# Performance work log

Hardware: AMD Instinct MI355X
Metric: run time of the kernel (lower is better)

The kernel has to match this reference:

```python
import jax, jax.numpy as jnp
import numpy as np

B = 4
MAX_N = 2048
D = 512
H = 8
HD = D // H
SRC_LENS = [2048, 1536, 1800, 1200]   # sum = 6584
REF_LENS = [1900, 2048, 1400, 1600]   # sum = 6948
NEG_INF = -1e9


def setup_inputs() -> dict:
    key = jax.random.key(0)
    ks = jax.random.split(key, 8)
    n_src, n_ref = sum(SRC_LENS), sum(REF_LENS)
    s = 0.02
    return {
        "feats_src": jax.random.normal(ks[0], (n_src, D), dtype=jnp.float32),
        "batch_src": jnp.asarray(np.repeat(np.arange(B), SRC_LENS), dtype=jnp.int32),
        "feats_ref": jax.random.normal(ks[1], (n_ref, D), dtype=jnp.float32),
        "batch_ref": jnp.asarray(np.repeat(np.arange(B), REF_LENS), dtype=jnp.int32),
        "w_in": jax.random.normal(ks[2], (3 * D, D), dtype=jnp.float32) * s,
        "b_in": jnp.zeros((3 * D,), dtype=jnp.float32),
        "w_out": jax.random.normal(ks[3], (D, D), dtype=jnp.float32) * s,
        "b_out": jnp.zeros((D,), dtype=jnp.float32),
        "gw1": jax.random.normal(ks[4], (D, D), dtype=jnp.float32) * s,
        "gb1": jnp.zeros((D,), dtype=jnp.float32),
        "gw2": jax.random.normal(ks[5], (1, D), dtype=jnp.float32) * s,
        "gb2": jnp.zeros((1,), dtype=jnp.float32),
    }


def _to_dense(feats, batch_idx):
    # sparse [N, D] (sorted batch indices) -> dense [B, MAX_N, D] + key_padding_mask
    n = feats.shape[0]
    counts = jax.ops.segment_sum(jnp.ones((n,), jnp.int32), batch_idx, num_segments=B)
    starts = jnp.concatenate([jnp.zeros((1,), jnp.int32), jnp.cumsum(counts)[:-1].astype(jnp.int32)])
    pos = jnp.arange(n, dtype=jnp.int32) - starts[batch_idx]  # position within batch
    dense = jnp.zeros((B, MAX_N, feats.shape[1]), feats.dtype).at[batch_idx, pos].set(feats)
    mask = jnp.arange(MAX_N)[None, :] >= counts[:, None]  # True = padding (key_padding_mask)
    return dense, mask, pos


def reference(feats_src, batch_src, feats_ref, batch_ref,
              w_in, b_in, w_out, b_out, gw1, gb1, gw2, gb2):
    d_src, mask_src, pos_src = _to_dense(feats_src, batch_src)
    d_ref, mask_ref, _ = _to_dense(feats_ref, batch_ref)

    # nn.MultiheadAttention (batch_first, eval mode): packed in_proj, scaled dot-product
    q = (d_src @ w_in[:D].T + b_in[:D]).reshape(B, MAX_N, H, HD)
    k = (d_ref @ w_in[D:2 * D].T + b_in[D:2 * D]).reshape(B, MAX_N, H, HD)
    v = (d_ref @ w_in[2 * D:].T + b_in[2 * D:]).reshape(B, MAX_N, H, HD)
    scores = jnp.einsum('bqhd,bkhd->bhqk', q * (HD ** -0.5), k)
    scores = jnp.where(mask_ref[:, None, None, :], NEG_INF, scores)
    attn = jax.nn.softmax(scores, axis=-1)
    ctx = jnp.einsum('bhqk,bkhd->bqhd', attn, v).reshape(B, MAX_N, D)
    d_aligned = ctx @ w_out.T + b_out

    # gate MLP: Linear -> ReLU -> Linear -> Sigmoid
    gate = jax.nn.sigmoid(jax.nn.relu(d_aligned @ gw1.T + gb1) @ gw2.T + gb2)  # [B, MAX_N, 1]
    d_out = d_src + gate * d_aligned

    # dense -> ragged: gather each token back to its flat slot
    out_flat = d_out[batch_src, pos_src]  # [N_src, D]
    return out_flat, gate
```

## Files before the change

### kernel.cpp

```cpp
#include <hip/hip_runtime.h>
#include <hip/hip_bf16.h>


typedef __bf16 bf16x8_t __attribute__((ext_vector_type(8)));
typedef __bf16 bf16x4_t __attribute__((ext_vector_type(4)));
typedef float f32x4_t __attribute__((ext_vector_type(4)));
typedef float f32x2_t __attribute__((ext_vector_type(2)));

__device__ inline bf16x8_t zero8() {
  bf16x8_t z;
#pragma unroll
  for (int t = 0; t < 8; ++t) z[t] = (__bf16)0.0f;
  return z;
}

__device__ __forceinline__ int sniff_f32(const void* w) {
  unsigned short u = ((const unsigned short*)w)[threadIdx.x & 63];
  return __ballot((u & 0x7F80) >= 0x3F80) != 0ULL;
}

__global__ void sentinel_k(float* out) {
  if (threadIdx.x == 0 && blockIdx.x == 0) out[0] = 1000.0f;
}

__global__ void cv_all(const void* w_in, const void* b_in, const void* w_out,
                       const void* b_out, const void* gw1, const void* gb1,
                       const void* gw2, const void* gb2,
                       __hip_bfloat16* __restrict__ ws) {
  int f = sniff_f32(w_in);
  const size_t F_W_IN = 16, F_B_IN = 786448, F_W_OUT = 787984, F_B_OUT = 1050128,
               F_GW1 = 1050640, F_GB1 = 1312784, F_GW2 = 1313296, F_GB2 = 1313808;
  const int total = 1313793;
  for (int g = blockIdx.x * 256 + threadIdx.x; g < total; g += gridDim.x * 256) {
    const void* src;
    size_t dst;
    int i;
    if (g < 786432) { src = w_in; dst = F_W_IN; i = g; }
    else if (g < 787968) { src = b_in; dst = F_B_IN; i = g - 786432; }
    else if (g < 1050112) { src = w_out; dst = F_W_OUT; i = g - 787968; }
    else if (g < 1050624) { src = b_out; dst = F_B_OUT; i = g - 1050112; }
    else if (g < 1312768) { src = gw1; dst = F_GW1; i = g - 1050624; }
    else if (g < 1313280) { src = gb1; dst = F_GB1; i = g - 1312768; }
    else if (g < 1313792) { src = gw2; dst = F_GW2; i = g - 1313280; }
    else { src = gb2; dst = F_GB2; i = g - 1313792; }
    ws[dst + i] = f ? __float2bfloat16(((const float*)src)[i])
                    : ((const __hip_bfloat16*)src)[i];
  }
}

template <bool AF32>
__global__ __launch_bounds__(256) void gemm128(
    const void* __restrict__ A_, long aoff, const __hip_bfloat16* __restrict__ Bt,
    const __hip_bfloat16* __restrict__ bias, __hip_bfloat16* __restrict__ C,
    int M, int K, int lda, int ldb, int ldc, float cscale, int relu,
    const void* snf) {
  __shared__ __bf16 As[128][64];
  __shared__ __bf16 Bs[128][64];
  int f = 0;
  if constexpr (AF32) f = sniff_f32(snf);
  int tid = threadIdx.x, lane = tid & 63, wave = tid >> 6;
  int wm = wave >> 1, wn = wave & 1;
  int l15 = lane & 15, quad = lane >> 4;
  int bm = blockIdx.x * 128, bn = blockIdx.y * 128;

  f32x4_t acc[4][4];
#pragma unroll
  for (int i = 0; i < 4; ++i)
#pragma unroll
    for (int j = 0; j < 4; ++j)
#pragma unroll
      for (int r = 0; r < 4; ++r) acc[i][j][r] = 0.f;

  bf16x8_t ra[4], rb[4];
  f32x4_t raf[4][2];

  auto gload = [&](int k0) {
#pragma unroll
    for (int s = 0; s < 4; ++s) {
      int id = s * 256 + tid;
      int row = id >> 3, col = (id & 7) * 8;
      int arow = bm + row;
      if (AF32 && f) {
        if (arow < M) {
          const float* p = (const float*)A_ + aoff + (size_t)arow * lda + k0 + col;
          raf[s][0] = *reinterpret_cast<const f32x4_t*>(p);
          raf[s][1] = *reinterpret_cast<const f32x4_t*>(p + 4);
        } else {
#pragma unroll
          for (int e = 0; e < 4; ++e) { raf[s][0][e] = 0.f; raf[s][1][e] = 0.f; }
        }
      } else {
        ra[s] = (arow < M)
                    ? *reinterpret_cast<const bf16x8_t*>((const __hip_bfloat16*)A_ + aoff +
                                                         (size_t)arow * lda + k0 + col)
                    : zero8();
      }
      rb[s] = *reinterpret_cast<const bf16x8_t*>(Bt + (size_t)(bn + row) * ldb + k0 + col);
    }
  };
  auto stage = [&]() {
#pragma unroll
    for (int s = 0; s < 4; ++s) {
      int id = s * 256 + tid;
      int row = id >> 3, col = (id & 7) * 8;
      if (AF32 && f) {
        bf16x8_t t;
#pragma unroll
        for (int e = 0; e < 4; ++e) {
          t[e] = (__bf16)raf[s][0][e];
          t[4 + e] = (__bf16)raf[s][1][e];
        }
        *reinterpret_cast<bf16x8_t*>(&As[row][col]) = t;
      } else {
        *reinterpret_cast<bf16x8_t*>(&As[row][col]) = ra[s];
      }
      *reinterpret_cast<bf16x8_t*>(&Bs[row][col]) = rb[s];
    }
  };

  int nk = K >> 6;
  gload(0);
  for (int it = 0; it < nk; ++it) {
    stage();
    __syncthreads();
    if (it + 1 < nk) gload((it + 1) * 64);
#pragma unroll
    for (int ks = 0; ks < 2; ++ks) {
      bf16x8_t af[4], bfv[4];
#pragma unroll
      for (int i = 0; i < 4; ++i)
        af[i] = *reinterpret_cast<const bf16x8_t*>(
            &As[wm * 64 + i * 16 + l15][ks * 32 + quad * 8]);
#pragma unroll
      for (int j = 0; j < 4; ++j)
        bfv[j] = *reinterpret_cast<const bf16x8_t*>(
            &Bs[wn * 64 + j * 16 + l15][ks * 32 + quad * 8]);
#pragma unroll
      for (int i = 0; i < 4; ++i)
#pragma unroll
        for (int j = 0; j < 4; ++j)
          acc[i][j] = __builtin_amdgcn_mfma_f32_16x16x32_bf16(af[i], bfv[j], acc[i][j], 0, 0, 0);
    }
    __syncthreads();
  }

#pragma unroll
  for (int i = 0; i < 4; ++i)
#pragma unroll
    for (int j = 0; j < 4; ++j) {
      int col = bn + wn * 64 + j * 16 + l15;
      float bv = __bfloat162float(bias[col]);
#pragma unroll
      for (int r = 0; r < 4; ++r) {
        int row = bm + wm * 64 + i * 16 + quad * 4 + r;
        if (row < M) {
          float v = (acc[i][j][r] + bv) * cscale;
          if (relu) v = fmaxf(v, 0.f);
          C[(size_t)row * ldc + col] = __float2bfloat16(v);
        }
      }
    }
}

__global__ __launch_bounds__(256) void gemm128_pv(
    const __hip_bfloat16* __restrict__ P0, const __hip_bfloat16* __restrict__ P1,
    const float* __restrict__ L, const __hip_bfloat16* __restrict__ Bt,
    const __hip_bfloat16* __restrict__ bias, __hip_bfloat16* __restrict__ C,
    int M) {
  __shared__ __bf16 As[128][64];
  __shared__ __bf16 Bs[128][64];
  int tid = threadIdx.x, lane = tid & 63, wave = tid >> 6;
  int wm = wave >> 1, wn = wave & 1;
  int l15 = lane & 15, quad = lane >> 4;
  int bm = blockIdx.x * 128, bn = blockIdx.y * 128;

  f32x4_t acc[4][4];
#pragma unroll
  for (int i = 0; i < 4; ++i)
#pragma unroll
    for (int j = 0; j < 4; ++j)
#pragma unroll
      for (int r = 0; r < 4; ++r) acc[i][j][r] = 0.f;

  bf16x8_t rp0[4], rp1[4], rb[4];
  f32x2_t rl[4];

  auto gload = [&](int k0) {
    int h = k0 >> 6;
#pragma unroll
    for (int s = 0; s < 4; ++s) {
      int id = s * 256 + tid;
      int row = id >> 3, col = (id & 7) * 8;
      int arow = bm + row;
      if (arow < M) {
        size_t off = (size_t)arow * 512 + k0 + col;
        rp0[s] = *reinterpret_cast<const bf16x8_t*>(P0 + off);
        rp1[s] = *reinterpret_cast<const bf16x8_t*>(P1 + off);
        rl[s] = *reinterpret_cast<const f32x2_t*>(&L[((size_t)arow * 8 + h) * 2]);
      } else {
        rp0[s] = zero8();
        rp1[s] = zero8();
        rl[s][0] = 1.f;
        rl[s][1] = 0.f;
      }
      rb[s] = *reinterpret_cast<const bf16x8_t*>(Bt + (size_t)(bn + row) * 512 + k0 + col);
    }
  };
  auto stage = [&]() {
#pragma unroll
    for (int s = 0; s < 4; ++s) {
      int id = s * 256 + tid;
      int row = id >> 3, col = (id & 7) * 8;
      float sc = 1.0f / (rl[s][0] + rl[s][1]);
      float w0 = rl[s][0] * sc, w1 = rl[s][1] * sc;
      bf16x8_t t;
#pragma unroll
      for (int e = 0; e < 8; ++e)
        t[e] = (__bf16)(w0 * (float)rp0[s][e] + w1 * (float)rp1[s][e]);
      *reinterpret_cast<bf16x8_t*>(&As[row][col]) = t;
      *reinterpret_cast<bf16x8_t*>(&Bs[row][col]) = rb[s];
    }
  };

  gload(0);
  for (int it = 0; it < 8; ++it) {
    stage();
    __syncthreads();
    if (it + 1 < 8) gload((it + 1) * 64);
#pragma unroll
    for (int ks = 0; ks < 2; ++ks) {
      bf16x8_t af[4], bfv[4];
#pragma unroll
      for (int i = 0; i < 4; ++i)
        af[i] = *reinterpret_cast<const bf16x8_t*>(
            &As[wm * 64 + i * 16 + l15][ks * 32 + quad * 8]);
#pragma unroll
      for (int j = 0; j < 4; ++j)
        bfv[j] = *reinterpret_cast<const bf16x8_t*>(
            &Bs[wn * 64 + j * 16 + l15][ks * 32 + quad * 8]);
#pragma unroll
      for (int i = 0; i < 4; ++i)
#pragma unroll
        for (int j = 0; j < 4; ++j)
          acc[i][j] = __builtin_amdgcn_mfma_f32_16x16x32_bf16(af[i], bfv[j], acc[i][j], 0, 0, 0);
    }
    __syncthreads();
  }

#pragma unroll
  for (int i = 0; i < 4; ++i)
#pragma unroll
    for (int j = 0; j < 4; ++j) {
      int col = bn + wn * 64 + j * 16 + l15;
      float bv = __bfloat162float(bias[col]);
#pragma unroll
      for (int r = 0; r < 4; ++r) {
        int row = bm + wm * 64 + i * 16 + quad * 4 + r;
        if (row < M)
          C[(size_t)row * 512 + col] = __float2bfloat16(acc[i][j][r] + bv);
      }
    }
}

__device__ __forceinline__ void flash_core(
    const __hip_bfloat16* __restrict__ Qb, const __hip_bfloat16* __restrict__ KVb,
    __hip_bfloat16* __restrict__ OUTb, float* __restrict__ LPb, int nsrc, int nref,
    int qt, int kt0, int ktNfull, int do_tail,
    __bf16 (&VtL)[2][64][72], __bf16 (&PL)[4][32][72]) {
  int h = blockIdx.y;
  int tid = threadIdx.x, lane = tid & 63, wave = tid >> 6;
  int l15 = lane & 15, quad = lane >> 4;
  int Mb = nsrc + 1;
  int qbase = qt * 128 + wave * 32;

  bf16x8_t qfr[2][2];
#pragma unroll
  for (int g = 0; g < 2; ++g) {
    int qrow = qbase + g * 16 + l15;
#pragma unroll
    for (int ks = 0; ks < 2; ++ks)
      qfr[g][ks] = (qrow < nsrc)
                       ? *reinterpret_cast<const bf16x8_t*>(
                             Qb + (size_t)qrow * 512 + h * 64 + ks * 32 + quad * 8)
                       : zero8();
  }

  f32x4_t O[2][4];
#pragma unroll
  for (int g = 0; g < 2; ++g)
#pragma unroll
    for (int j = 0; j < 4; ++j)
#pragma unroll
      for (int r = 0; r < 4; ++r) O[g][j][r] = 0.f;
  float lsum[2] = {0.f, 0.f};

  bf16x8_t kf[8], v0, v1;
  auto loadK = [&](int k0) {
#pragma unroll
    for (int j = 0; j < 4; ++j) {
      const __hip_bfloat16* kp =
          KVb + (size_t)(k0 + j * 16 + l15) * 1024 + h * 64 + quad * 8;
      kf[j * 2] = *reinterpret_cast<const bf16x8_t*>(kp);
      kf[j * 2 + 1] = *reinterpret_cast<const bf16x8_t*>(kp + 32);
    }
  };
  auto loadV = [&](int k0) {
    const __hip_bfloat16* vp = KVb + (size_t)(k0 + lane) * 1024 + 512 + h * 64 + wave * 16;
    v0 = *reinterpret_cast<const bf16x8_t*>(vp);
    v1 = *reinterpret_cast<const bf16x8_t*>(vp + 8);
  };

  int nit = ktNfull - kt0;
  if (nit > 0) {
    loadK(kt0 * 64);
    loadV(kt0 * 64);
  }

  for (int it = 0; it < nit; ++it) {
    int k0 = (kt0 + it) * 64;
    __bf16(*Vt)[72] = VtL[it & 1];
#pragma unroll
    for (int e = 0; e < 8; ++e) {
      Vt[wave * 16 + e][lane] = v0[e];
      Vt[wave * 16 + 8 + e][lane] = v1[e];
    }
    if (it + 1 < nit) loadV(k0 + 64);

    f32x4_t St[2][4];
#pragma unroll
    for (int g = 0; g < 2; ++g)
#pragma unroll
      for (int j = 0; j < 4; ++j)
#pragma unroll
        for (int r = 0; r < 4; ++r) St[g][j][r] = 0.f;
#pragma unroll
    for (int g = 0; g < 2; ++g)
#pragma unroll
      for (int j = 0; j < 4; ++j)
#pragma unroll
        for (int ks = 0; ks < 2; ++ks)
          St[g][j] = __builtin_amdgcn_mfma_f32_16x16x32_bf16(kf[j * 2 + ks], qfr[g][ks],
                                                             St[g][j], 0, 0, 0);
    if (it + 1 < nit) loadK(k0 + 64);

#pragma unroll
    for (int g = 0; g < 2; ++g)
#pragma unroll
      for (int j = 0; j < 4; ++j) {
        bf16x4_t pk;
#pragma unroll
        for (int r = 0; r < 4; ++r) {
          float p = exp2f(St[g][j][r]);
          lsum[g] += p;
          pk[r] = (__bf16)p;
        }
        *reinterpret_cast<bf16x4_t*>(&PL[wave][g * 16 + l15][j * 16 + quad * 4]) = pk;
      }

    __syncthreads();

    bf16x8_t pa[2][2];
#pragma unroll
    for (int g = 0; g < 2; ++g)
#pragma unroll
      for (int ks = 0; ks < 2; ++ks)
        pa[g][ks] = *reinterpret_cast<const bf16x8_t*>(
            &PL[wave][g * 16 + l15][ks * 32 + quad * 8]);
#pragma unroll
    for (int j = 0; j < 4; ++j)
#pragma unroll
      for (int ks = 0; ks < 2; ++ks) {
        bf16x8_t vb =
            *reinterpret_cast<const bf16x8_t*>(&Vt[j * 16 + l15][ks * 32 + quad * 8]);
#pragma unroll
        for (int g = 0; g < 2; ++g)
          O[g][j] = __builtin_amdgcn_mfma_f32_16x16x32_bf16(pa[g][ks], vb, O[g][j], 0, 0, 0);
      }
  }

  if (do_tail) {
    int k0 = ktNfull * 64;
    __bf16(*Vt)[72] = VtL[nit & 1];
    {
      int kr = k0 + lane;
      const __hip_bfloat16* vp = KVb + (size_t)kr * 1024 + 512 + h * 64 + wave * 16;
      bf16x8_t t0 = (kr < nref) ? *reinterpret_cast<const bf16x8_t*>(vp) : zero8();
      bf16x8_t t1 = (kr < nref) ? *reinterpret_cast<const bf16x8_t*>(vp + 8) : zero8();
#pragma unroll
      for (int e = 0; e < 8; ++e) {
        Vt[wave * 16 + e][lane] = t0[e];
        Vt[wave * 16 + 8 + e][lane] = t1[e];
      }
    }
#pragma unroll
    for (int j = 0; j < 4; ++j) {
      int kcol = k0 + j * 16 + l15;
      const __hip_bfloat16* kp = KVb + (size_t)kcol * 1024 + h * 64 + quad * 8;
      kf[j * 2] = (kcol < nref) ? *reinterpret_cast<const bf16x8_t*>(kp) : zero8();
      kf[j * 2 + 1] = (kcol < nref) ? *reinterpret_cast<const bf16x8_t*>(kp + 32) : zero8();
    }
#pragma unroll
    for (int g = 0; g < 2; ++g) {
      f32x4_t St[4];
#pragma unroll
      for (int j = 0; j < 4; ++j)
#pragma unroll
        for (int r = 0; r < 4; ++r) St[j][r] = 0.f;
#pragma unroll
      for (int j = 0; j < 4; ++j)
#pragma unroll
        for (int ks = 0; ks < 2; ++ks)
          St[j] = __builtin_amdgcn_mfma_f32_16x16x32_bf16(kf[j * 2 + ks], qfr[g][ks],
                                                          St[j], 0, 0, 0);
#pragma unroll
      for (int j = 0; j < 4; ++j) {
        bf16x4_t pk;
#pragma unroll
        for (int r = 0; r < 4; ++r) {
          int kl = k0 + j * 16 + quad * 4 + r;
          float p = (kl < nref) ? exp2f(St[j][r]) : 0.f;
          lsum[g] += p;
          pk[r] = (__bf16)p;
        }
        *reinterpret_cast<bf16x4_t*>(&PL[wave][g * 16 + l15][j * 16 + quad * 4]) = pk;
      }
    }
    __syncthreads();
    bf16x8_t pa[2][2];
#pragma unroll
    for (int g = 0; g < 2; ++g)
#pragma unroll
      for (int ks = 0; ks < 2; ++ks)
        pa[g][ks] = *reinterpret_cast<const bf16x8_t*>(
            &PL[wave][g * 16 + l15][ks * 32 + quad * 8]);
#pragma unroll
    for (int j = 0; j < 4; ++j)
#pragma unroll
      for (int ks = 0; ks < 2; ++ks) {
        bf16x8_t vb =
            *reinterpret_cast<const bf16x8_t*>(&Vt[j * 16 + l15][ks * 32 + quad * 8]);
#pragma unroll
        for (int g = 0; g < 2; ++g)
          O[g][j] = __builtin_amdgcn_mfma_f32_16x16x32_bf16(pa[g][ks], vb, O[g][j], 0, 0, 0);
      }
  }

#pragma unroll
  for (int g = 0; g < 2; ++g) {
    lsum[g] += __shfl_xor(lsum[g], 16);
    lsum[g] += __shfl_xor(lsum[g], 32);
  }

  if (LPb && quad == 0) {
#pragma unroll
    for (int g = 0; g < 2; ++g) {
      int row = qbase + g * 16 + l15;
      if (row < Mb) LPb[((size_t)row * 8 + h) * 2] = lsum[g];
    }
  }

#pragma unroll
  for (int g = 0; g < 2; ++g)
#pragma unroll
    for (int r = 0; r < 4; ++r) {
      int row = qbase + g * 16 + quad * 4 + r;
      if (row < Mb) {
        float li = __shfl(lsum[g], quad * 4 + r);
        float inv = 1.0f / li;
#pragma unroll
        for (int j = 0; j < 4; ++j)
          OUTb[(size_t)row * 512 + h * 64 + j * 16 + l15] =
              __float2bfloat16(O[g][j][r] * inv);
      }
    }
}

__global__ __launch_bounds__(256) void flash_all(
    const __hip_bfloat16* __restrict__ Q, const __hip_bfloat16* __restrict__ KV,
    __hip_bfloat16* __restrict__ O0, __hip_bfloat16* __restrict__ O1,
    float* __restrict__ L, int nsplit) {
  const int TILE_START[4] = {0, 17, 30, 45};
  const int SRC_START[4] = {0, 2048, 3584, 5384};
  const int REF_START[4] = {0, 1900, 3948, 5348};
  const int SRC_LEN[4] = {2048, 1536, 1800, 1200};
  const int REF_LEN[4] = {1900, 2048, 1400, 1600};
  const int CS[4] = {0, 2049, 3586, 5387};
  __shared__ __bf16 VtL[2][64][72];
  __shared__ __bf16 PL[4][32][72];
  int bid = blockIdx.x;
  int b = (bid >= TILE_START[3]) ? 3 : (bid >= TILE_START[2]) ? 2 : (bid >= TILE_START[1]) ? 1 : 0;
  int qt = bid - TILE_START[b];
  int nref = REF_LEN[b];
  int full = nref >> 6, nkt = (nref + 63) >> 6, rem = nref & 63;
  int split = blockIdx.z;
  int kt0, ktN, tail;
  if (nsplit == 1) { kt0 = 0; ktN = full; tail = rem > 0; }
  else if (split == 0) { int half = nkt >> 1; kt0 = 0; ktN = half; tail = 0; }
  else { int half = nkt >> 1; kt0 = half; ktN = full; tail = rem > 0; }
  __hip_bfloat16* OUT = (nsplit == 1 || split == 0) ? O0 : O1;
  float* LP = (nsplit == 1) ? nullptr : (L + split + (size_t)CS[b] * 16);
  flash_core(Q + (size_t)SRC_START[b] * 512, KV + (size_t)REF_START[b] * 1024,
             OUT + (size_t)CS[b] * 512, LP, SRC_LEN[b], nref, qt, kt0, ktN, tail, VtL, PL);
}

__global__ __launch_bounds__(256) void flash_one(const __hip_bfloat16* __restrict__ Qb,
                                                 const __hip_bfloat16* __restrict__ KVb,
                                                 __hip_bfloat16* __restrict__ OUTb,
                                                 int nsrc, int nref) {
  __shared__ __bf16 VtL[2][64][72];
  __shared__ __bf16 PL[4][32][72];
  flash_core(Qb, KVb, OUTb, nullptr, nsrc, nref, blockIdx.x, 0, nref >> 6,
             (nref & 63) > 0, VtL, PL);
}

__global__ __launch_bounds__(256) void finalize_all(
    const void* __restrict__ src, const __hip_bfloat16* __restrict__ aligned,
    const __hip_bfloat16* __restrict__ hidden, const __hip_bfloat16* __restrict__ gw2,
    const __hip_bfloat16* __restrict__ gb2, void* __restrict__ out, const void* snf) {
  int f = sniff_f32(snf);
  int lane = threadIdx.x & 63;
  int r = blockIdx.x * 4 + (threadIdx.x >> 6);
  int b = (r >= 5387) ? 3 : (r >= 3586) ? 2 : (r >= 2049) ? 1 : 0;
  const int CS[4] = {0, 2049, 3586, 5387};
  const int NSRC[4] = {2048, 1536, 1800, 1200};
  int pos = r - CS[b];

  float zacc = 0.f;
  const __hip_bfloat16* hrow = hidden + (size_t)r * 512;
#pragma unroll
  for (int t = 0; t < 8; ++t) {
    int c = lane + (t << 6);
    zacc += __bfloat162float(hrow[c]) * __bfloat162float(gw2[c]);
  }
  for (int o = 32; o; o >>= 1) zacc += __shfl_xor(zacc, o);
  zacc += __bfloat162float(gb2[0]);
  float g = 1.f / (1.f + __expf(-zacc));

  const size_t GOFF = (size_t)6584 * 512;
  if (pos < NSRC[b]) {
    size_t ib = (size_t)(r - b) * 512;
    const __hip_bfloat16* arow = aligned + (size_t)r * 512;
#pragma unroll
    for (int t = 0; t < 8; ++t) {
      int c = lane + (t << 6);
      float sv = f ? ((const float*)src)[ib + c]
                   : __bfloat162float(((const __hip_bfloat16*)src)[ib + c]);
      float val = sv + g * __bfloat162float(arow[c]);
      if (f) ((float*)out)[ib + c] = val;
      else ((__hip_bfloat16*)out)[ib + c] = __float2bfloat16(val);
    }
    if (lane == 0) {
      size_t go = GOFF + b * 2048 + pos;
      if (f) ((float*)out)[go] = g;
      else ((__hip_bfloat16*)out)[go] = __float2bfloat16(g);
    }
  } else {
    for (int p = NSRC[b] + lane; p < 2048; p += 64) {
      size_t go = GOFF + b * 2048 + p;
      if (f) ((float*)out)[go] = g;
      else ((__hip_bfloat16*)out)[go] = __float2bfloat16(g);
    }
  }
}

__global__ __launch_bounds__(256) void finalize_b(
    const void* __restrict__ src, const __hip_bfloat16* __restrict__ alnb,
    const __hip_bfloat16* __restrict__ hidb, const __hip_bfloat16* __restrict__ gw2,
    const __hip_bfloat16* __restrict__ gb2, void* __restrict__ out,
    int b, int nsrc, int src_start, const void* snf) {
  int f = sniff_f32(snf);
  int lane = threadIdx.x & 63;
  int r = blockIdx.x * 4 + (threadIdx.x >> 6);
  if (r > nsrc) return;

  float zacc = 0.f;
  const __hip_bfloat16* hrow = hidb + (size_t)r * 512;
#pragma unroll
  for (int t = 0; t < 8; ++t) {
    int c = lane + (t << 6);
    zacc += __bfloat162float(hrow[c]) * __bfloat162float(gw2[c]);
  }
  for (int o = 32; o; o >>= 1) zacc += __shfl_xor(zacc, o);
  zacc += __bfloat162float(gb2[0]);
  float g = 1.f / (1.f + __expf(-zacc));

  const size_t GOFF = (size_t)6584 * 512;
  if (r < nsrc) {
    size_t ib = (size_t)(src_start + r) * 512;
    const __hip_bfloat16* arow = alnb + (size_t)r * 512;
#pragma unroll
    for (int t = 0; t < 8; ++t) {
      int c = lane + (t << 6);
      float sv = f ? ((const float*)src)[ib + c]
                   : __bfloat162float(((const __hip_bfloat16*)src)[ib + c]);
      float val = sv + g * __bfloat162float(arow[c]);
      if (f) ((float*)out)[ib + c] = val;
      else ((__hip_bfloat16*)out)[ib + c] = __float2bfloat16(val);
    }
    if (lane == 0) {
      size_t go = GOFF + b * 2048 + r;
      if (f) ((float*)out)[go] = g;
      else ((__hip_bfloat16*)out)[go] = __float2bfloat16(g);
    }
  } else {
    for (int p = nsrc + lane; p < 2048; p += 64) {
      size_t go = GOFF + b * 2048 + p;
      if (f) ((float*)out)[go] = g;
      else ((__hip_bfloat16*)out)[go] = __float2bfloat16(g);
    }
  }
}

extern "C" void kernel_launch(void* const* d_in, const int* in_sizes, int n_in,
                              void* d_out, int out_size, void* d_ws, size_t ws_size,
                              hipStream_t stream) {
  (void)in_sizes; (void)n_in; (void)out_size;
  const void* feats_src = d_in[0];
  const void* feats_ref = d_in[2];
  const void* w_in = d_in[4];
  const void* b_in = d_in[5];
  const void* w_out = d_in[6];
  const void* b_out = d_in[7];
  const void* gw1 = d_in[8];
  const void* gb1 = d_in[9];
  const void* gw2 = d_in[10];
  const void* gb2 = d_in[11];

  const size_t F_W_IN = 16, F_B_IN = 786448, F_W_OUT = 787984, F_B_OUT = 1050128,
               F_GW1 = 1050640, F_GB1 = 1312784, F_GW2 = 1313296, F_GB2 = 1313808,
               A0 = 1313824;
  const size_t NEED_A2 = 2 * 22139936;
  const size_t NEED_A = 2 * 15178784;
  const size_t NEED_B = 2 * (A0 + 4259840);
  const float CQ = 0.18033688011112042f;

  if (ws_size < NEED_B) {
    sentinel_k<<<1, 64, 0, stream>>>((float*)d_out);
    return;
  }

  __hip_bfloat16* ws = (__hip_bfloat16*)d_ws;
  cv_all<<<dim3(1024), dim3(256), 0, stream>>>(w_in, b_in, w_out, b_out, gw1, gb1, gw2,
                                               gb2, ws);

  const int SRC_LEN[4] = {2048, 1536, 1800, 1200};
  const int REF_LEN[4] = {1900, 2048, 1400, 1600};
  const int SRC_START[4] = {0, 2048, 3584, 5384};
  const int REF_START[4] = {0, 1900, 3948, 5348};
  dim3 blk(256);

  if (ws_size >= NEED_A) {
    __hip_bfloat16* R1 = ws + A0;
    __hip_bfloat16* R2 = R1 + 3375104;
    __hip_bfloat16* R3 = R2 + 7114752;
    gemm128<true><<<dim3(52, 4), blk, 0, stream>>>(feats_src, 0, ws + F_W_IN,
                                                   ws + F_B_IN, R1, 6584, 512, 512, 512,
                                                   512, CQ, 0, w_in);
    gemm128<true><<<dim3(55, 8), blk, 0, stream>>>(feats_ref, 0, ws + F_W_IN + 262144,
                                                   ws + F_B_IN + 512, R2, 6948, 512, 512,
                                                   512, 1024, 1.0f, 0, w_in);
    if (ws_size >= NEED_A2) {
      __hip_bfloat16* P0 = R3 + 3375104;
      __hip_bfloat16* P1 = P0 + 3375104;
      float* L = (float*)(ws + 21928992);
      flash_all<<<dim3(55, 8, 2), blk, 0, stream>>>(R1, R2, P0, P1, L, 2);
      gemm128_pv<<<dim3(52, 4), blk, 0, stream>>>(P0, P1, L, ws + F_W_OUT, ws + F_B_OUT,
                                                  R1, 6588);
    } else {
      flash_all<<<dim3(55, 8, 1), blk, 0, stream>>>(R1, R2, R3, nullptr, nullptr, 1);
      gemm128<false><<<dim3(52, 4), blk, 0, stream>>>(R3, 0, ws + F_W_OUT, ws + F_B_OUT,
                                                      R1, 6588, 512, 512, 512, 512, 1.0f,
                                                      0, nullptr);
    }
    gemm128<false><<<dim3(52, 4), blk, 0, stream>>>(R1, 0, ws + F_GW1, ws + F_GB1, R3,
                                                    6588, 512, 512, 512, 512, 1.0f, 1,
                                                    nullptr);
    finalize_all<<<dim3(1647), blk, 0, stream>>>(feats_src, R1, R3, ws + F_GW2,
                                                 ws + F_GB2, d_out, w_in);
  } else {
    __hip_bfloat16* W2 = ws + A0;
    __hip_bfloat16* W1 = W2 + 2097152;
    __hip_bfloat16* W3 = W1 + 1081344;
    for (int b = 0; b < 4; ++b) {
      int nsrc = SRC_LEN[b], nref = REF_LEN[b];
      gemm128<true><<<dim3((nsrc + 127) / 128, 4), blk, 0, stream>>>(
          feats_src, (long)SRC_START[b] * 512, ws + F_W_IN, ws + F_B_IN, W1, nsrc, 512,
          512, 512, 512, CQ, 0, w_in);
      gemm128<true><<<dim3((nref + 127) / 128, 8), blk, 0, stream>>>(
          feats_ref, (long)REF_START[b] * 512, ws + F_W_IN + 262144, ws + F_B_IN + 512,
          W2, nref, 512, 512, 512, 1024, 1.0f, 0, w_in);
      flash_one<<<dim3((nsrc + 128) / 128, 8), blk, 0, stream>>>(W1, W2, W3, nsrc, nref);
      gemm128<false><<<dim3((nsrc + 128) / 128, 4), blk, 0, stream>>>(
          W3, 0, ws + F_W_OUT, ws + F_B_OUT, W1, nsrc + 1, 512, 512, 512, 512, 1.0f, 0,
          nullptr);
      gemm128<false><<<dim3((nsrc + 128) / 128, 4), blk, 0, stream>>>(
          W1, 0, ws + F_GW1, ws + F_GB1, W3, nsrc + 1, 512, 512, 512, 512, 1.0f, 1,
          nullptr);
      finalize_b<<<dim3((nsrc + 4) / 4), blk, 0, stream>>>(
          feats_src, W1, W3, ws + F_GW2, ws + F_GB2, d_out, b, nsrc, SRC_START[b], w_in);
    }
  }
}
```

Before: 261.4 us.

## Emit V pre-transposed from KV projection to drop LDS transpose in flash

The K/V projection GEMM now writes K row-major and V transposed per batch (head-dim rows, padded key columns) by swapping operand roles for the V half. The flash attention kernel then loads V fragments directly from global memory into registers instead of staging a transpose through shared memory. This removes the V LDS buffer and a per-iteration block barrier. In exchange it adds strided transposed stores in the GEMM epilogue, extra per-lane global loads of V, and more workspace for the padded layout.

```diff
diff --git a/kernel.cpp b/kernel.cpp
--- a/kernel.cpp
+++ b/kernel.cpp
@@ -162,6 +162,157 @@
     }
 }
 
+__device__ __forceinline__ void gemm_kv_core(
+    const void* __restrict__ A_, long aoffB, int f,
+    const __hip_bfloat16* __restrict__ W, const __hip_bfloat16* __restrict__ bias,
+    __hip_bfloat16* __restrict__ KVKb, __hip_bfloat16* __restrict__ VTb,
+    int nref, int npadT, int mt, int bn) {
+  __shared__ __bf16 As[128][64];
+  __shared__ __bf16 Bs[128][64];
+  int tid = threadIdx.x, lane = tid & 63, wave = tid >> 6;
+  int wm = wave >> 1, wn = wave & 1;
+  int l15 = lane & 15, quad = lane >> 4;
+
+  f32x4_t acc[4][4];
+#pragma unroll
+  for (int i = 0; i < 4; ++i)
+#pragma unroll
+    for (int j = 0; j < 4; ++j)
+#pragma unroll
+      for (int r = 0; r < 4; ++r) acc[i][j][r] = 0.f;
+
+  bf16x8_t ra[4], rb[4];
+  f32x4_t raf[4][2];
+  auto gload = [&](int k0) {
+#pragma unroll
+    for (int s = 0; s < 4; ++s) {
+      int id = s * 256 + tid;
+      int row = id >> 3, col = (id & 7) * 8;
+      int arow = mt + row;
+      if (f) {
+        if (arow < nref) {
+          const float* p = (const float*)A_ + aoffB + (size_t)arow * 512 + k0 + col;
+          raf[s][0] = *reinterpret_cast<const f32x4_t*>(p);
+          raf[s][1] = *reinterpret_cast<const f32x4_t*>(p + 4);
+        } else {
+#pragma unroll
+          for (int e = 0; e < 4; ++e) { raf[s][0][e] = 0.f; raf[s][1][e] = 0.f; }
+        }
+      } else {
+        ra[s] = (arow < nref)
+                    ? *reinterpret_cast<const bf16x8_t*>((const __hip_bfloat16*)A_ + aoffB +
+                                                         (size_t)arow * 512 + k0 + col)
+                    : zero8();
+      }
+      rb[s] = *reinterpret_cast<const bf16x8_t*>(W + (size_t)(bn + row) * 512 + k0 + col);
+    }
+  };
+  auto stage = [&]() {
+#pragma unroll
+    for (int s = 0; s < 4; ++s) {
+      int id = s * 256 + tid;
+      int row = id >> 3, col = (id & 7) * 8;
+      if (f) {
+        bf16x8_t t;
+#pragma unroll
+        for (int e = 0; e < 4; ++e) {
+          t[e] = (__bf16)raf[s][0][e];
+          t[4 + e] = (__bf16)raf[s][1][e];
+        }
+        *reinterpret_cast<bf16x8_t*>(&As[row][col]) = t;
+      } else {
+        *reinterpret_cast<bf16x8_t*>(&As[row][col]) = ra[s];
+      }
+      *reinterpret_cast<bf16x8_t*>(&Bs[row][col]) = rb[s];
+    }
+  };
+
+  int vhalf = (bn >= 512);
+  gload(0);
+  for (int it = 0; it < 8; ++it) {
+    stage();
+    __syncthreads();
+    if (it + 1 < 8) gload((it + 1) * 64);
+#pragma unroll
+    for (int ks = 0; ks < 2; ++ks) {
+      bf16x8_t af[4], bfv[4];
+#pragma unroll
+      for (int i = 0; i < 4; ++i)
+        af[i] = vhalf ? *reinterpret_cast<const bf16x8_t*>(
+                            &Bs[wm * 64 + i * 16 + l15][ks * 32 + quad * 8])
+                      : *reinterpret_cast<const bf16x8_t*>(
+                            &As[wm * 64 + i * 16 + l15][ks * 32 + quad * 8]);
+#pragma unroll
+      for (int j = 0; j < 4; ++j)
+        bfv[j] = vhalf ? *reinterpret_cast<const bf16x8_t*>(
+                             &As[wn * 64 + j * 16 + l15][ks * 32 + quad * 8])
+                       : *reinterpret_cast<const bf16x8_t*>(
+                             &Bs[wn * 64 + j * 16 + l15][ks * 32 + quad * 8]);
+#pragma unroll
+      for (int i = 0; i < 4; ++i)
+#pragma unroll
+        for (int j = 0; j < 4; ++j)
+          acc[i][j] = __builtin_amdgcn_mfma_f32_16x16x32_bf16(af[i], bfv[j], acc[i][j], 0, 0, 0);
+    }
+    __syncthreads();
+  }
+
+  if (!vhalf) {
+#pragma unroll
+    for (int i = 0; i < 4; ++i)
+#pragma unroll
+      for (int j = 0; j < 4; ++j) {
+        int col = bn + wn * 64 + j * 16 + l15;
+        float bv = __bfloat162float(bias[col]);
+#pragma unroll
+        for (int r = 0; r < 4; ++r) {
+          int m = mt + wm * 64 + i * 16 + quad * 4 + r;
+          if (m < nref) KVKb[(size_t)m * 512 + col] = __float2bfloat16(acc[i][j][r] + bv);
+        }
+      }
+  } else {
+#pragma unroll
+    for (int i = 0; i < 4; ++i)
+#pragma unroll
+      for (int r = 0; r < 4; ++r) {
+        int nloc = wm * 64 + i * 16 + quad * 4 + r;
+        int nV = bn - 512 + nloc;
+        float bv = __bfloat162float(bias[bn + nloc]);
+#pragma unroll
+        for (int j = 0; j < 4; ++j) {
+          int k = mt + wn * 64 + j * 16 + l15;
+          VTb[(size_t)nV * npadT + k] = __float2bfloat16(acc[i][j][r] + bv);
+        }
+      }
+  }
+}
+
+__global__ __launch_bounds__(256) void gemm_kv4(
+    const void* __restrict__ feats_ref, const __hip_bfloat16* __restrict__ W,
+    const __hip_bfloat16* __restrict__ bias, __hip_bfloat16* __restrict__ KVK,
+    __hip_bfloat16* __restrict__ VT, const void* snf) {
+  const int KVT[4] = {0, 15, 31, 42};
+  const int REF_START[4] = {0, 1900, 3948, 5348};
+  const int REF_LEN[4] = {1900, 2048, 1400, 1600};
+  const int NPADT[4] = {1920, 2048, 1408, 1664};
+  const int VTOFF[4] = {0, 983040, 2031616, 2752512};
+  int bid = blockIdx.x;
+  int b = (bid >= KVT[3]) ? 3 : (bid >= KVT[2]) ? 2 : (bid >= KVT[1]) ? 1 : 0;
+  int f = sniff_f32(snf);
+  gemm_kv_core(feats_ref, (long)REF_START[b] * 512, f, W, bias,
+               KVK + (size_t)REF_START[b] * 512, VT + VTOFF[b], REF_LEN[b], NPADT[b],
+               (bid - KVT[b]) * 128, blockIdx.y * 128);
+}
+
+__global__ __launch_bounds__(256) void gemm_kv1(
+    const void* __restrict__ feats_ref, long aoffB, const __hip_bfloat16* __restrict__ W,
+    const __hip_bfloat16* __restrict__ bias, __hip_bfloat16* __restrict__ KVKb,
+    __hip_bfloat16* __restrict__ VTb, int nref, int npadT, const void* snf) {
+  int f = sniff_f32(snf);
+  gemm_kv_core(feats_ref, aoffB, f, W, bias, KVKb, VTb, nref, npadT,
+               blockIdx.x * 128, blockIdx.y * 128);
+}
+
 __global__ __launch_bounds__(256) void gemm128_pv(
     const __hip_bfloat16* __restrict__ P0, const __hip_bfloat16* __restrict__ P1,
     const float* __restrict__ L, const __hip_bfloat16* __restrict__ Bt,
@@ -263,15 +414,16 @@
 }
 
 __device__ __forceinline__ void flash_core(
-    const __hip_bfloat16* __restrict__ Qb, const __hip_bfloat16* __restrict__ KVb,
+    const __hip_bfloat16* __restrict__ Qb, const __hip_bfloat16* __restrict__ Kb,
+    const __hip_bfloat16* __restrict__ VTb, int npadT,
     __hip_bfloat16* __restrict__ OUTb, float* __restrict__ LPb, int nsrc, int nref,
-    int qt, int kt0, int ktNfull, int do_tail,
-    __bf16 (&VtL)[2][64][72], __bf16 (&PL)[4][32][72]) {
+    int qt, int kt0, int ktNfull, int do_tail, __bf16 (&PL)[4][32][72]) {
   int h = blockIdx.y;
   int tid = threadIdx.x, lane = tid & 63, wave = tid >> 6;
   int l15 = lane & 15, quad = lane >> 4;
   int Mb = nsrc + 1;
   int qbase = qt * 128 + wave * 32;
+  const __hip_bfloat16* Vh = VTb + (size_t)h * 64 * npadT;
 
   bf16x8_t qfr[2][2];
 #pragma unroll
@@ -294,20 +446,22 @@
       for (int r = 0; r < 4; ++r) O[g][j][r] = 0.f;
   float lsum[2] = {0.f, 0.f};
 
-  bf16x8_t kf[8], v0, v1;
+  bf16x8_t kf[8], vb[8];
   auto loadK = [&](int k0) {
 #pragma unroll
     for (int j = 0; j < 4; ++j) {
-      const __hip_bfloat16* kp =
-          KVb + (size_t)(k0 + j * 16 + l15) * 1024 + h * 64 + quad * 8;
+      const __hip_bfloat16* kp = Kb + (size_t)(k0 + j * 16 + l15) * 512 + h * 64 + quad * 8;
       kf[j * 2] = *reinterpret_cast<const bf16x8_t*>(kp);
       kf[j * 2 + 1] = *reinterpret_cast<const bf16x8_t*>(kp + 32);
     }
   };
   auto loadV = [&](int k0) {
-    const __hip_bfloat16* vp = KVb + (size_t)(k0 + lane) * 1024 + 512 + h * 64 + wave * 16;
-    v0 = *reinterpret_cast<const bf16x8_t*>(vp);
-    v1 = *reinterpret_cast<const bf16x8_t*>(vp + 8);
+#pragma unroll
+    for (int j = 0; j < 4; ++j) {
+      const __hip_bfloat16* vp = Vh + (size_t)(j * 16 + l15) * npadT + k0 + quad * 8;
+      vb[j * 2] = *reinterpret_cast<const bf16x8_t*>(vp);
+      vb[j * 2 + 1] = *reinterpret_cast<const bf16x8_t*>(vp + 32);
+    }
   };
 
   int nit = ktNfull - kt0;
@@ -318,14 +472,6 @@
 
   for (int it = 0; it < nit; ++it) {
     int k0 = (kt0 + it) * 64;
-    __bf16(*Vt)[72] = VtL[it & 1];
-#pragma unroll
-    for (int e = 0; e < 8; ++e) {
-      Vt[wave * 16 + e][lane] = v0[e];
-      Vt[wave * 16 + 8 + e][lane] = v1[e];
-    }
-    if (it + 1 < nit) loadV(k0 + 64);
-
     f32x4_t St[2][4];
 #pragma unroll
     for (int g = 0; g < 2; ++g)
@@ -357,8 +503,6 @@
         *reinterpret_cast<bf16x4_t*>(&PL[wave][g * 16 + l15][j * 16 + quad * 4]) = pk;
       }
 
-    __syncthreads();
-
     bf16x8_t pa[2][2];
 #pragma unroll
     for (int g = 0; g < 2; ++g)
@@ -369,63 +513,53 @@
 #pragma unroll
     for (int j = 0; j < 4; ++j)
 #pragma unroll
-      for (int ks = 0; ks < 2; ++ks) {
-        bf16x8_t vb =
-            *reinterpret_cast<const bf16x8_t*>(&Vt[j * 16 + l15][ks * 32 + quad * 8]);
+      for (int ks = 0; ks < 2; ++ks)
 #pragma unroll
         for (int g = 0; g < 2; ++g)
-          O[g][j] = __builtin_amdgcn_mfma_f32_16x16x32_bf16(pa[g][ks], vb, O[g][j], 0, 0, 0);
-      }
+          O[g][j] = __builtin_amdgcn_mfma_f32_16x16x32_bf16(pa[g][ks], vb[j * 2 + ks],
+                                                            O[g][j], 0, 0, 0);
+    if (it + 1 < nit) loadV(k0 + 64);
   }
 
   if (do_tail) {
     int k0 = ktNfull * 64;
-    __bf16(*Vt)[72] = VtL[nit & 1];
-    {
-      int kr = k0 + lane;
-      const __hip_bfloat16* vp = KVb + (size_t)kr * 1024 + 512 + h * 64 + wave * 16;
-      bf16x8_t t0 = (kr < nref) ? *reinterpret_cast<const bf16x8_t*>(vp) : zero8();
-      bf16x8_t t1 = (kr < nref) ? *reinterpret_cast<const bf16x8_t*>(vp + 8) : zero8();
-#pragma unroll
-      for (int e = 0; e < 8; ++e) {
-        Vt[wave * 16 + e][lane] = t0[e];
-        Vt[wave * 16 + 8 + e][lane] = t1[e];
-      }
-    }
 #pragma unroll
     for (int j = 0; j < 4; ++j) {
       int kcol = k0 + j * 16 + l15;
-      const __hip_bfloat16* kp = KVb + (size_t)kcol * 1024 + h * 64 + quad * 8;
+      const __hip_bfloat16* kp = Kb + (size_t)kcol * 512 + h * 64 + quad * 8;
       kf[j * 2] = (kcol < nref) ? *reinterpret_cast<const bf16x8_t*>(kp) : zero8();
       kf[j * 2 + 1] = (kcol < nref) ? *reinterpret_cast<const bf16x8_t*>(kp + 32) : zero8();
     }
-#pragma unroll
-    for (int g = 0; g < 2; ++g) {
-      f32x4_t St[4];
+    loadV(k0);
+    f32x4_t St[2][4];
+#pragma unroll
+    for (int g = 0; g < 2; ++g)
 #pragma unroll
       for (int j = 0; j < 4; ++j)
 #pragma unroll
-        for (int r = 0; r < 4; ++r) St[j][r] = 0.f;
+        for (int r = 0; r < 4; ++r) St[g][j][r] = 0.f;
+#pragma unroll
+    for (int g = 0; g < 2; ++g)
 #pragma unroll
       for (int j = 0; j < 4; ++j)
 #pragma unroll
         for (int ks = 0; ks < 2; ++ks)
-          St[j] = __builtin_amdgcn_mfma_f32_16x16x32_bf16(kf[j * 2 + ks], qfr[g][ks],
-                                                          St[j], 0, 0, 0);
+          St[g][j] = __builtin_amdgcn_mfma_f32_16x16x32_bf16(kf[j * 2 + ks], qfr[g][ks],
+                                                             St[g][j], 0, 0, 0);
+#pragma unroll
+    for (int g = 0; g < 2; ++g)
 #pragma unroll
       for (int j = 0; j < 4; ++j) {
         bf16x4_t pk;
 #pragma unroll
         for (int r = 0; r < 4; ++r) {
           int kl = k0 + j * 16 + quad * 4 + r;
-          float p = (kl < nref) ? exp2f(St[j][r]) : 0.f;
+          float p = (kl < nref) ? exp2f(St[g][j][r]) : 0.f;
           lsum[g] += p;
           pk[r] = (__bf16)p;
         }
         *reinterpret_cast<bf16x4_t*>(&PL[wave][g * 16 + l15][j * 16 + quad * 4]) = pk;
       }
-    }
-    __syncthreads();
     bf16x8_t pa[2][2];
 #pragma unroll
     for (int g = 0; g < 2; ++g)
@@ -436,13 +570,11 @@
 #pragma unroll
     for (int j = 0; j < 4; ++j)
 #pragma unroll
-      for (int ks = 0; ks < 2; ++ks) {
-        bf16x8_t vb =
-            *reinterpret_cast<const bf16x8_t*>(&Vt[j * 16 + l15][ks * 32 + quad * 8]);
+      for (int ks = 0; ks < 2; ++ks)
 #pragma unroll
         for (int g = 0; g < 2; ++g)
-          O[g][j] = __builtin_amdgcn_mfma_f32_16x16x32_bf16(pa[g][ks], vb, O[g][j], 0, 0, 0);
-      }
+          O[g][j] = __builtin_amdgcn_mfma_f32_16x16x32_bf16(pa[g][ks], vb[j * 2 + ks],
+                                                            O[g][j], 0, 0, 0);
   }
 
 #pragma unroll
@@ -476,16 +608,17 @@
 }
 
 __global__ __launch_bounds__(256) void flash_all(
-    const __hip_bfloat16* __restrict__ Q, const __hip_bfloat16* __restrict__ KV,
-    __hip_bfloat16* __restrict__ O0, __hip_bfloat16* __restrict__ O1,
-    float* __restrict__ L, int nsplit) {
+    const __hip_bfloat16* __restrict__ Q, const __hip_bfloat16* __restrict__ KVK,
+    const __hip_bfloat16* __restrict__ VT, __hip_bfloat16* __restrict__ O0,
+    __hip_bfloat16* __restrict__ O1, float* __restrict__ L, int nsplit) {
   const int TILE_START[4] = {0, 17, 30, 45};
   const int SRC_START[4] = {0, 2048, 3584, 5384};
   const int REF_START[4] = {0, 1900, 3948, 5348};
   const int SRC_LEN[4] = {2048, 1536, 1800, 1200};
   const int REF_LEN[4] = {1900, 2048, 1400, 1600};
+  const int NPADT[4] = {1920, 2048, 1408, 1664};
+  const int VTOFF[4] = {0, 983040, 2031616, 2752512};
   const int CS[4] = {0, 2049, 3586, 5387};
-  __shared__ __bf16 VtL[2][64][72];
   __shared__ __bf16 PL[4][32][72];
   int bid = blockIdx.x;
   int b = (bid >= TILE_START[3]) ? 3 : (bid >= TILE_START[2]) ? 2 : (bid >= TILE_START[1]) ? 1 : 0;
@@ -499,18 +632,18 @@
   else { int half = nkt >> 1; kt0 = half; ktN = full; tail = rem > 0; }
   __hip_bfloat16* OUT = (nsplit == 1 || split == 0) ? O0 : O1;
   float* LP = (nsplit == 1) ? nullptr : (L + split + (size_t)CS[b] * 16);
-  flash_core(Q + (size_t)SRC_START[b] * 512, KV + (size_t)REF_START[b] * 1024,
-             OUT + (size_t)CS[b] * 512, LP, SRC_LEN[b], nref, qt, kt0, ktN, tail, VtL, PL);
-}
-
-__global__ __launch_bounds__(256) void flash_one(const __hip_bfloat16* __restrict__ Qb,
-                                                 const __hip_bfloat16* __restrict__ KVb,
-                                                 __hip_bfloat16* __restrict__ OUTb,
-                                                 int nsrc, int nref) {
-  __shared__ __bf16 VtL[2][64][72];
+  flash_core(Q + (size_t)SRC_START[b] * 512, KVK + (size_t)REF_START[b] * 512,
+             VT + VTOFF[b], NPADT[b], OUT + (size_t)CS[b] * 512, LP, SRC_LEN[b], nref,
+             qt, kt0, ktN, tail, PL);
+}
+
+__global__ __launch_bounds__(256) void flash_one(
+    const __hip_bfloat16* __restrict__ Qb, const __hip_bfloat16* __restrict__ KVKb,
+    const __hip_bfloat16* __restrict__ VTb, int npadT,
+    __hip_bfloat16* __restrict__ OUTb, int nsrc, int nref) {
   __shared__ __bf16 PL[4][32][72];
-  flash_core(Qb, KVb, OUTb, nullptr, nsrc, nref, blockIdx.x, 0, nref >> 6,
-             (nref & 63) > 0, VtL, PL);
+  flash_core(Qb, KVKb, VTb, npadT, OUTb, nullptr, nsrc, nref, blockIdx.x, 0, nref >> 6,
+             (nref & 63) > 0, PL);
 }
 
 __global__ __launch_bounds__(256) void finalize_all(
@@ -629,8 +762,15 @@
   const size_t F_W_IN = 16, F_B_IN = 786448, F_W_OUT = 787984, F_B_OUT = 1050128,
                F_GW1 = 1050640, F_GB1 = 1312784, F_GW2 = 1313296, F_GB2 = 1313808,
                A0 = 1313824;
-  const size_t NEED_A2 = 2 * 22139936;
-  const size_t NEED_A = 2 * 15178784;
+  const size_t OFF_R1 = A0;
+  const size_t OFF_KVK = OFF_R1 + 3375104;
+  const size_t OFF_VT = OFF_KVK + 3557376;
+  const size_t OFF_R3 = OFF_VT + 3604480;
+  const size_t OFF_P0 = OFF_R3 + 3375104;
+  const size_t OFF_P1 = OFF_P0 + 3375104;
+  const size_t OFF_L = OFF_P1 + 3375104;
+  const size_t NEED_A2 = 2 * (OFF_L + 210816);
+  const size_t NEED_A = 2 * OFF_P0;
   const size_t NEED_B = 2 * (A0 + 4259840);
   const float CQ = 0.18033688011112042f;
 
@@ -647,27 +787,28 @@
   const int REF_LEN[4] = {1900, 2048, 1400, 1600};
   const int SRC_START[4] = {0, 2048, 3584, 5384};
   const int REF_START[4] = {0, 1900, 3948, 5348};
+  const int NPADT[4] = {1920, 2048, 1408, 1664};
   dim3 blk(256);
 
   if (ws_size >= NEED_A) {
-    __hip_bfloat16* R1 = ws + A0;
-    __hip_bfloat16* R2 = R1 + 3375104;
-    __hip_bfloat16* R3 = R2 + 7114752;
+    __hip_bfloat16* R1 = ws + OFF_R1;
+    __hip_bfloat16* KVK = ws + OFF_KVK;
+    __hip_bfloat16* VT = ws + OFF_VT;
+    __hip_bfloat16* R3 = ws + OFF_R3;
     gemm128<true><<<dim3(52, 4), blk, 0, stream>>>(feats_src, 0, ws + F_W_IN,
                                                    ws + F_B_IN, R1, 6584, 512, 512, 512,
                                                    512, CQ, 0, w_in);
-    gemm128<true><<<dim3(55, 8), blk, 0, stream>>>(feats_ref, 0, ws + F_W_IN + 262144,
-                                                   ws + F_B_IN + 512, R2, 6948, 512, 512,
-                                                   512, 1024, 1.0f, 0, w_in);
+    gemm_kv4<<<dim3(55, 8), blk, 0, stream>>>(feats_ref, ws + F_W_IN + 262144,
+                                              ws + F_B_IN + 512, KVK, VT, w_in);
     if (ws_size >= NEED_A2) {
-      __hip_bfloat16* P0 = R3 + 3375104;
-      __hip_bfloat16* P1 = P0 + 3375104;
-      float* L = (float*)(ws + 21928992);
-      flash_all<<<dim3(55, 8, 2), blk, 0, stream>>>(R1, R2, P0, P1, L, 2);
+      __hip_bfloat16* P0 = ws + OFF_P0;
+      __hip_bfloat16* P1 = ws + OFF_P1;
+      float* L = (float*)(ws + OFF_L);
+      flash_all<<<dim3(55, 8, 2), blk, 0, stream>>>(R1, KVK, VT, P0, P1, L, 2);
       gemm128_pv<<<dim3(52, 4), blk, 0, stream>>>(P0, P1, L, ws + F_W_OUT, ws + F_B_OUT,
                                                   R1, 6588);
     } else {
-      flash_all<<<dim3(55, 8, 1), blk, 0, stream>>>(R1, R2, R3, nullptr, nullptr, 1);
+      flash_all<<<dim3(55, 8, 1), blk, 0, stream>>>(R1, KVK, VT, R3, nullptr, nullptr, 1);
       gemm128<false><<<dim3(52, 4), blk, 0, stream>>>(R3, 0, ws + F_W_OUT, ws + F_B_OUT,
                                                       R1, 6588, 512, 512, 512, 512, 1.0f,
                                                       0, nullptr);
@@ -678,18 +819,20 @@
     finalize_all<<<dim3(1647), blk, 0, stream>>>(feats_src, R1, R3, ws + F_GW2,
                                                  ws + F_GB2, d_out, w_in);
   } else {
-    __hip_bfloat16* W2 = ws + A0;
-    __hip_bfloat16* W1 = W2 + 2097152;
+    __hip_bfloat16* KVKb = ws + A0;
+    __hip_bfloat16* VTb = KVKb + 1048576;
+    __hip_bfloat16* W1 = VTb + 1048576;
     __hip_bfloat16* W3 = W1 + 1081344;
     for (int b = 0; b < 4; ++b) {
-      int nsrc = SRC_LEN[b], nref = REF_LEN[b];
+      int nsrc = SRC_LEN[b], nref = REF_LEN[b], npadT = NPADT[b];
       gemm128<true><<<dim3((nsrc + 127) / 128, 4), blk, 0, stream>>>(
           feats_src, (long)SRC_START[b] * 512, ws + F_W_IN, ws + F_B_IN, W1, nsrc, 512,
           512, 512, 512, CQ, 0, w_in);
-      gemm128<true><<<dim3((nref + 127) / 128, 8), blk, 0, stream>>>(
+      gemm_kv1<<<dim3(npadT / 128, 8), blk, 0, stream>>>(
           feats_ref, (long)REF_START[b] * 512, ws + F_W_IN + 262144, ws + F_B_IN + 512,
-          W2, nref, 512, 512, 512, 1024, 1.0f, 0, w_in);
-      flash_one<<<dim3((nsrc + 128) / 128, 8), blk, 0, stream>>>(W1, W2, W3, nsrc, nref);
+          KVKb, VTb, nref, npadT, w_in);
+      flash_one<<<dim3((nsrc + 128) / 128, 8), blk, 0, stream>>>(W1, KVKb, VTb, npadT,
+                                                                 W3, nsrc, nref);
       gemm128<false><<<dim3((nsrc + 128) / 128, 4), blk, 0, stream>>>(
           W3, 0, ws + F_W_OUT, ws + F_B_OUT, W1, nsrc + 1, 512, 512, 512, 512, 1.0f, 0,
           nullptr);
```

After: 289.3 us. 10.6% more time.
